# Kernel tuning notes

Measured on AMD Instinct MI355X. Metric: run time of the kernel, lower is better.

## Reference

```python
import jax, jax.numpy as jnp
import numpy as np

LOC_SIZE, TIM_SIZE = 50000, 48
LOC_EMB, TIM_EMB = 512, 32
IN = LOC_EMB + TIM_EMB  # 544
HID = 1024
SEQ, TGT = 4096, 1024


def _gru(x, Wih, Whh, bih, bhh):
    """PyTorch-convention GRU over [S, IN] -> [S, HID], h0 = 0."""
    gi = x @ Wih.T + bih  # [S, 3H] precomputed input gates
    H = Whh.shape[1]

    def step(h, gi_t):
        gh = Whh @ h + bhh
        i_r, i_z, i_n = jnp.split(gi_t, 3)
        h_r, h_z, h_n = jnp.split(gh, 3)
        r = jax.nn.sigmoid(i_r + h_r)
        z = jax.nn.sigmoid(i_z + h_z)
        n = jnp.tanh(i_n + r * h_n)
        h_new = (1.0 - z) * n + z * h
        return h_new, h_new

    _, hs = jax.lax.scan(step, jnp.zeros((H,), x.dtype), gi)
    return hs


def setup_inputs() -> dict:
    key = jax.random.key(0)
    ks = jax.random.split(key, 16)
    s = 0.02
    inp = {
        "loc": jax.random.randint(ks[0], (SEQ, 1), 0, LOC_SIZE),
        "tim": jax.random.randint(ks[1], (SEQ, 1), 0, TIM_SIZE),
        "target_len": TGT,
        "emb_loc": jax.random.normal(ks[2], (LOC_SIZE, LOC_EMB), jnp.float32) * s,
        "emb_tim": jax.random.normal(ks[3], (TIM_SIZE, TIM_EMB), jnp.float32) * s,
        "Wih_enc": jax.random.normal(ks[4], (3 * HID, IN), jnp.float32) * s,
        "Whh_enc": jax.random.normal(ks[5], (3 * HID, HID), jnp.float32) * s,
        "bih_enc": jnp.zeros((3 * HID,), jnp.float32),
        "bhh_enc": jnp.zeros((3 * HID,), jnp.float32),
        "Wih_dec": jax.random.normal(ks[6], (3 * HID, IN), jnp.float32) * s,
        "Whh_dec": jax.random.normal(ks[7], (3 * HID, HID), jnp.float32) * s,
        "bih_dec": jnp.zeros((3 * HID,), jnp.float32),
        "bhh_dec": jnp.zeros((3 * HID,), jnp.float32),
        "W_fc": jax.random.normal(ks[8], (LOC_SIZE, 2 * HID), jnp.float32) * s,
        "b_fc": jnp.zeros((LOC_SIZE,), jnp.float32),
    }
    return inp


def reference(loc, tim, target_len, emb_loc, emb_tim,
              Wih_enc, Whh_enc, bih_enc, bhh_enc,
              Wih_dec, Whh_dec, bih_dec, bhh_dec,
              W_fc, b_fc):
    # embeddings, batch dim of 1 squeezed: [S, IN]
    x = jnp.concatenate([emb_loc[loc[:, 0]], emb_tim[tim[:, 0]]], axis=1)
    # dropout is identity in eval mode
    hidden_history = _gru(x[:-target_len], Wih_enc, Whh_enc, bih_enc, bhh_enc)  # [S-T, H]
    hidden_state = _gru(x[-target_len:], Wih_dec, Whh_dec, bih_dec, bhh_dec)    # [T, H]
    # 'dot' attention: fused GEMM + row softmax (replaces the O(T*S) python loop)
    energies = hidden_state @ hidden_history.T                                   # [T, S-T]
    attn_weights = jax.nn.softmax(energies, axis=-1)
    context = attn_weights @ hidden_history                                      # [T, H]
    out = jnp.concatenate([hidden_state, context], axis=1)                       # [T, 2H]
    y = out @ W_fc.T + b_fc                                                      # [T, LOC_SIZE]
    return jax.nn.log_softmax(y, axis=-1)
```

## Files before the change

kernel.cpp:

```cpp
#include <hip/hip_runtime.h>
#include <hip/hip_bf16.h>
#include <cstdint>

typedef __attribute__((ext_vector_type(4))) float floatx4;
typedef __attribute__((ext_vector_type(8))) __bf16 bf16x8;
typedef __attribute__((ext_vector_type(4))) __bf16 bf16x4;
typedef unsigned long long u64t;

#define HID    1024
#define SEQ    4096
#define TGT    1024
#define ENC_T  3072
#define IN_DIM 544
#define NCLS   50000

__global__ __launch_bounds__(128) void embed_kernel(
    const int* __restrict__ loc, const int* __restrict__ tim,
    const float* __restrict__ el, const float* __restrict__ et,
    float* __restrict__ x) {
  int row = blockIdx.x, t = threadIdx.x;
  int li = loc[row], ti = tim[row];
  float4 v = *(const float4*)(el + (size_t)li * 512 + t * 4);
  *(float4*)(x + (size_t)row * IN_DIM + t * 4) = v;
  if (t < 8) {
    float4 w = *(const float4*)(et + (size_t)ti * 32 + t * 4);
    *(float4*)(x + (size_t)row * IN_DIM + 512 + t * 4) = w;
  }
}

#define BK  64
#define LDT 72

__global__ __launch_bounds__(256) void gemm_nt(
    const float* __restrict__ A, int lda,
    const float* __restrict__ B, int ldb,
    float* __restrict__ C, int ldc,
    const float* __restrict__ bias,
    int M, int N, int K) {
  __shared__ __bf16 As[128 * LDT];
  __shared__ __bf16 Bs[128 * LDT];
  const int tid = threadIdx.x;
  const int bm = blockIdx.x * 128, bn = blockIdx.y * 128;
  const int wave = tid >> 6, lane = tid & 63;
  const int wm = (wave & 1) * 64, wn = (wave >> 1) * 64;
  const int fr = lane & 15;
  const int kq = (lane >> 4) * 8;

  floatx4 acc[4][4];
#pragma unroll
  for (int i = 0; i < 4; i++)
#pragma unroll
    for (int j = 0; j < 4; j++) acc[i][j] = (floatx4){0.f, 0.f, 0.f, 0.f};

  const int nkt = (K + BK - 1) / BK;
  for (int kt = 0; kt < nkt; ++kt) {
    const int k0 = kt * BK;
#pragma unroll
    for (int i = 0; i < 8; i++) {
      int flat = tid + i * 256;
      int r = flat >> 4;
      int c4 = (flat & 15) * 4;
      float4 va = {0, 0, 0, 0}, vb = {0, 0, 0, 0};
      if (k0 + c4 < K) {
        va = *(const float4*)(A + (size_t)(bm + r) * lda + k0 + c4);
        if (bn + r < N) vb = *(const float4*)(B + (size_t)(bn + r) * ldb + k0 + c4);
      }
      *(bf16x4*)(As + r * LDT + c4) =
          (bf16x4){(__bf16)va.x, (__bf16)va.y, (__bf16)va.z, (__bf16)va.w};
      *(bf16x4*)(Bs + r * LDT + c4) =
          (bf16x4){(__bf16)vb.x, (__bf16)vb.y, (__bf16)vb.z, (__bf16)vb.w};
    }
    __syncthreads();
#pragma unroll
    for (int kh = 0; kh < 2; ++kh) {
      const int kf = kh * 32 + kq;
      bf16x8 af[4], bfr[4];
#pragma unroll
      for (int i = 0; i < 4; i++) {
        af[i]  = *(const bf16x8*)(As + (wm + i * 16 + fr) * LDT + kf);
        bfr[i] = *(const bf16x8*)(Bs + (wn + i * 16 + fr) * LDT + kf);
      }
#pragma unroll
      for (int mi = 0; mi < 4; mi++)
#pragma unroll
        for (int ni = 0; ni < 4; ni++)
          acc[mi][ni] = __builtin_amdgcn_mfma_f32_16x16x32_bf16(
              af[mi], bfr[ni], acc[mi][ni], 0, 0, 0);
    }
    __syncthreads();
  }

  const int em = (lane >> 4) * 4;
#pragma unroll
  for (int mi = 0; mi < 4; mi++) {
#pragma unroll
    for (int ni = 0; ni < 4; ni++) {
      int gn = bn + wn + ni * 16 + fr;
      if (gn < N) {
        float bv = bias ? bias[gn] : 0.f;
        int gm = bm + wm + mi * 16 + em;
#pragma unroll
        for (int r2 = 0; r2 < 4; r2++)
          C[(size_t)(gm + r2) * ldc + gn] = acc[mi][ni][r2] + bv;
      }
    }
  }
}

#define SC_WGS 128

__device__ __forceinline__ float flo(unsigned int u) {
  return __builtin_bit_cast(float, u << 16);
}
__device__ __forceinline__ float fhi(unsigned int u) {
  return __builtin_bit_cast(float, u & 0xffff0000u);
}

__global__ __launch_bounds__(256) void scan_kernel(
    const float* __restrict__ Whh_e, const float* __restrict__ bhh_e, const float* __restrict__ gi_e,
    const float* __restrict__ Whh_d, const float* __restrict__ bhh_d, const float* __restrict__ gi_d,
    float* __restrict__ Hh, float* __restrict__ HhT, float* __restrict__ outcat,
    unsigned int* __restrict__ hbuf_e, unsigned int* __restrict__ hbuf_d) {
  const bool enc = blockIdx.x < SC_WGS;
  const int wid = enc ? blockIdx.x : (blockIdx.x - SC_WGS);
  const int T = enc ? ENC_T : TGT;
  const float* Whh = enc ? Whh_e : Whh_d;
  const float* bhh = enc ? bhh_e : bhh_d;
  const float* gi  = enc ? gi_e : gi_d;
  unsigned int* hbuf = enc ? hbuf_e : hbuf_d;

  __shared__ uint2 wrz[8 * 512];
  __shared__ unsigned int wnn[8 * 512];
  const int tid = threadIdx.x;

  for (int i = tid; i < 8 * 512; i += 256) {
    int el = i >> 9, k2 = i & 511;
    int rb = wid * 8 + el;
    float2 w0 = *(const float2*)(Whh + (size_t)(0 * HID + rb) * HID + 2 * k2);
    float2 w1 = *(const float2*)(Whh + (size_t)(1 * HID + rb) * HID + 2 * k2);
    float2 w2 = *(const float2*)(Whh + (size_t)(2 * HID + rb) * HID + 2 * k2);
    unsigned int p0 = (unsigned int)__builtin_bit_cast(unsigned short, (__bf16)w0.x) |
                      ((unsigned int)__builtin_bit_cast(unsigned short, (__bf16)w0.y) << 16);
    unsigned int p1 = (unsigned int)__builtin_bit_cast(unsigned short, (__bf16)w1.x) |
                      ((unsigned int)__builtin_bit_cast(unsigned short, (__bf16)w1.y) << 16);
    unsigned int p2 = (unsigned int)__builtin_bit_cast(unsigned short, (__bf16)w2.x) |
                      ((unsigned int)__builtin_bit_cast(unsigned short, (__bf16)w2.y) << 16);
    wrz[i] = make_uint2(p0, p1);
    wnn[i] = p2;
  }
  __syncthreads();

  const int l = tid & 63;
  const int w = tid >> 6;
  const int le0 = w * 2, le1 = le0 + 1;
  const int e0 = wid * 8 + le0;

  float bq = 0.f;
  if (l < 3) bq = bhh[l * HID + e0];
  else if (l >= 4 && l < 7) bq = bhh[(l - 4) * HID + (e0 + 1)];

  const uint2* wrz0 = wrz + le0 * 512;
  const uint2* wrz1 = wrz + le1 * 512;
  const unsigned int* wnn0 = wnn + le0 * 512;
  const unsigned int* wnn1 = wnn + le1 * 512;

  float h_own = 0.f;
  long budget = 1L << 21;

  for (int t = 0; t < T; ++t) {
    float gval = 0.f;
    if (l < 3) gval = gi[(size_t)t * 3072 + l * HID + e0];
    else if (l >= 4 && l < 7) gval = gi[(size_t)t * 3072 + (l - 4) * HID + (e0 + 1)];

    const u64t* hp = (const u64t*)(hbuf + ((t + 1) & 1) * HID);
    const unsigned int tlo = (unsigned int)t;
    float ar0, az0, an0, ar1, az1, an1;
    for (;;) {
      u64t hv[8];
#pragma unroll
      for (int j = 0; j < 8; ++j)
        hv[j] = __hip_atomic_load(hp + l + 64 * j, __ATOMIC_RELAXED, __HIP_MEMORY_SCOPE_AGENT);
      bool ok = true;
      ar0 = az0 = an0 = ar1 = az1 = an1 = 0.f;
#pragma unroll
      for (int j = 0; j < 8; ++j) {
        unsigned int w0 = (unsigned int)hv[j];
        unsigned int w1 = (unsigned int)(hv[j] >> 32);
        ok &= ((w0 >> 16) >= tlo) & ((w1 >> 16) >= tlo);
        float h0 = flo(w0);
        float h1 = flo(w1);
        int i = l + 64 * j;
        uint2 u0 = wrz0[i];
        unsigned int n0 = wnn0[i];
        uint2 u1 = wrz1[i];
        unsigned int n1 = wnn1[i];
        ar0 += flo(u0.x) * h0 + fhi(u0.x) * h1;
        az0 += flo(u0.y) * h0 + fhi(u0.y) * h1;
        an0 += flo(n0) * h0 + fhi(n0) * h1;
        ar1 += flo(u1.x) * h0 + fhi(u1.x) * h1;
        az1 += flo(u1.y) * h0 + fhi(u1.y) * h1;
        an1 += flo(n1) * h0 + fhi(n1) * h1;
      }
      if (__all(ok)) break;
      if (--budget < 0) break;
    }
#pragma unroll
    for (int o = 32; o; o >>= 1) {
      ar0 += __shfl_xor(ar0, o); az0 += __shfl_xor(az0, o); an0 += __shfl_xor(an0, o);
      ar1 += __shfl_xor(ar1, o); az1 += __shfl_xor(az1, o); an1 += __shfl_xor(an1, o);
    }
    int base = (l & 1) * 4;
    float i_r = __shfl(gval, base + 0);
    float i_z = __shfl(gval, base + 1);
    float i_n = __shfl(gval, base + 2);
    float b_r = __shfl(bq, base + 0);
    float b_z = __shfl(bq, base + 1);
    float b_n = __shfl(bq, base + 2);
    if (l < 2) {
      float sr = l ? ar1 : ar0;
      float sz = l ? az1 : az0;
      float sn = l ? an1 : an0;
      int e = e0 + l;
      float r = 1.f / (1.f + expf(-(i_r + sr + b_r)));
      float z = 1.f / (1.f + expf(-(i_z + sz + b_z)));
      float nn2 = tanhf(i_n + r * (sn + b_n));
      float hnew = (1.f - z) * nn2 + z * h_own;
      h_own = hnew;
      unsigned int pk = ((unsigned int)(t + 1) << 16) |
                        (unsigned int)__builtin_bit_cast(unsigned short, (__bf16)hnew);
      __hip_atomic_store(&hbuf[(t & 1) * HID + e], pk,
                         __ATOMIC_RELAXED, __HIP_MEMORY_SCOPE_AGENT);
      if (enc) {
        Hh[(size_t)t * HID + e] = hnew;
        HhT[(size_t)e * ENC_T + t] = hnew;
      } else {
        outcat[(size_t)t * 2048 + e] = hnew;
      }
    }
  }
}

__device__ __forceinline__ float wave_max(float v) {
#pragma unroll
  for (int o = 32; o; o >>= 1) v = fmaxf(v, __shfl_xor(v, o));
  return v;
}
__device__ __forceinline__ float wave_sum(float v) {
#pragma unroll
  for (int o = 32; o; o >>= 1) v += __shfl_xor(v, o);
  return v;
}

__global__ __launch_bounds__(256) void softmax_kernel(float* __restrict__ E) {
  __shared__ float red[4];
  int row = blockIdx.x;
  float* p = E + (size_t)row * ENC_T;
  int tid = threadIdx.x, wave = tid >> 6;
  float v[12];
  float m = -3.4e38f;
#pragma unroll
  for (int j = 0; j < 12; j++) { v[j] = p[tid + j * 256]; m = fmaxf(m, v[j]); }
  m = wave_max(m);
  if ((tid & 63) == 0) red[wave] = m;
  __syncthreads();
  m = fmaxf(fmaxf(red[0], red[1]), fmaxf(red[2], red[3]));
  __syncthreads();
  float s = 0.f;
#pragma unroll
  for (int j = 0; j < 12; j++) { v[j] = expf(v[j] - m); s += v[j]; }
  s = wave_sum(s);
  if ((tid & 63) == 0) red[wave] = s;
  __syncthreads();
  s = red[0] + red[1] + red[2] + red[3];
  float inv = 1.f / s;
#pragma unroll
  for (int j = 0; j < 12; j++) p[tid + j * 256] = v[j] * inv;
}

__global__ __launch_bounds__(256) void lse_kernel(const float* __restrict__ Y,
                                                  float* __restrict__ lse) {
  __shared__ float red[4];
  int row = blockIdx.x;
  const float* p = Y + (size_t)row * NCLS;
  int tid = threadIdx.x, wave = tid >> 6;
  float m = -3.4e38f;
  for (int c = tid; c < NCLS; c += 256) m = fmaxf(m, p[c]);
  m = wave_max(m);
  if ((tid & 63) == 0) red[wave] = m;
  __syncthreads();
  m = fmaxf(fmaxf(red[0], red[1]), fmaxf(red[2], red[3]));
  __syncthreads();
  float s = 0.f;
  for (int c = tid; c < NCLS; c += 256) s += expf(p[c] - m);
  s = wave_sum(s);
  if ((tid & 63) == 0) red[wave] = s;
  __syncthreads();
  if (tid == 0) lse[row] = m + logf(red[0] + red[1] + red[2] + red[3]);
}

__global__ __launch_bounds__(256) void sub_kernel(float* __restrict__ Y,
                                                  const float* __restrict__ lse) {
  const unsigned total = (unsigned)TGT * (NCLS / 4);
  unsigned stride = gridDim.x * 256;
  for (unsigned i = blockIdx.x * 256 + threadIdx.x; i < total; i += stride) {
    unsigned row = i / (NCLS / 4);
    float l = lse[row];
    float4 v = ((float4*)Y)[i];
    v.x -= l; v.y -= l; v.z -= l; v.w -= l;
    ((float4*)Y)[i] = v;
  }
}

extern "C" void kernel_launch(void* const* d_in, const int* in_sizes, int n_in,
                              void* d_out, int out_size, void* d_ws, size_t ws_size,
                              hipStream_t stream) {
  const int*   loc     = (const int*)d_in[0];
  const int*   tim     = (const int*)d_in[1];
  const float* emb_loc = (const float*)d_in[3];
  const float* emb_tim = (const float*)d_in[4];
  const float* Wih_e   = (const float*)d_in[5];
  const float* Whh_e   = (const float*)d_in[6];
  const float* bih_e   = (const float*)d_in[7];
  const float* bhh_e   = (const float*)d_in[8];
  const float* Wih_d   = (const float*)d_in[9];
  const float* Whh_d   = (const float*)d_in[10];
  const float* bih_d   = (const float*)d_in[11];
  const float* bhh_d   = (const float*)d_in[12];
  const float* W_fc    = (const float*)d_in[13];
  const float* b_fc    = (const float*)d_in[14];
  float* out = (float*)d_out;

  float* ws = (float*)d_ws;
  unsigned int* hbuf_e = (unsigned int*)ws;
  unsigned int* hbuf_d = (unsigned int*)(ws + 2048);
  float* lse    = ws + 4096;
  float* x      = ws + 5120;
  float* gi_e   = x + (size_t)SEQ * IN_DIM;
  float* gi_d   = gi_e + (size_t)ENC_T * 3072;
  float* Hh     = gi_d + (size_t)TGT * 3072;
  float* HhT    = Hh + (size_t)ENC_T * HID;
  float* outcat = HhT + (size_t)HID * ENC_T;
  float* energ  = outcat + (size_t)TGT * 2048;

  hipMemsetAsync(d_ws, 0, 4096 * sizeof(float), stream);

  embed_kernel<<<SEQ, 128, 0, stream>>>(loc, tim, emb_loc, emb_tim, x);

  gemm_nt<<<dim3(ENC_T / 128, 3072 / 128), 256, 0, stream>>>(
      x, IN_DIM, Wih_e, IN_DIM, gi_e, 3072, bih_e, ENC_T, 3072, IN_DIM);
  gemm_nt<<<dim3(TGT / 128, 3072 / 128), 256, 0, stream>>>(
      x + (size_t)ENC_T * IN_DIM, IN_DIM, Wih_d, IN_DIM, gi_d, 3072, bih_d, TGT, 3072, IN_DIM);

  scan_kernel<<<2 * SC_WGS, 256, 0, stream>>>(Whh_e, bhh_e, gi_e, Whh_d, bhh_d, gi_d,
                                              Hh, HhT, outcat, hbuf_e, hbuf_d);

  gemm_nt<<<dim3(TGT / 128, ENC_T / 128), 256, 0, stream>>>(
      outcat, 2048, Hh, HID, energ, ENC_T, nullptr, TGT, ENC_T, HID);
  softmax_kernel<<<TGT, 256, 0, stream>>>(energ);
  gemm_nt<<<dim3(TGT / 128, HID / 128), 256, 0, stream>>>(
      energ, ENC_T, HhT, ENC_T, outcat + HID, 2048, nullptr, TGT, HID, ENC_T);

  gemm_nt<<<dim3(TGT / 128, (NCLS + 127) / 128), 256, 0, stream>>>(
      outcat, 2048, W_fc, 2048, out, NCLS, b_fc, TGT, NCLS, 2048);

  lse_kernel<<<TGT, 256, 0, stream>>>(out, lse);
  sub_kernel<<<4096, 256, 0, stream>>>(out, lse);
}
```

Baseline: 16.99 ms.

## Add aggregator workgroup publishing per-step epoch counter for scan synchronization

Adds an extra workgroup to the persistent GRU scan kernel. It polls the tagged hidden-state buffers, computes the minimum completed step across all elements, and publishes it to 16 replicated epoch counters. Scan workgroups then spin on a single epoch word before loading the full hidden vector, instead of repeatedly reloading all 8 tagged words per lane. This aims to cut global polling traffic and contention, but adds a hop of latency per step through the aggregator. It also relies on the extra block being co-resident with the others.

Measured after the change: 14.20 ms. -16.4%, faster.

```diff
diff --git a/kernel.cpp b/kernel.cpp
--- a/kernel.cpp
+++ b/kernel.cpp
@@ -120,7 +120,43 @@
     const float* __restrict__ Whh_e, const float* __restrict__ bhh_e, const float* __restrict__ gi_e,
     const float* __restrict__ Whh_d, const float* __restrict__ bhh_d, const float* __restrict__ gi_d,
     float* __restrict__ Hh, float* __restrict__ HhT, float* __restrict__ outcat,
-    unsigned int* __restrict__ hbuf_e, unsigned int* __restrict__ hbuf_d) {
+    unsigned int* __restrict__ hbuf_e, unsigned int* __restrict__ hbuf_d,
+    unsigned int* __restrict__ epoch) {
+  const int tid = threadIdx.x;
+
+  if (blockIdx.x == 2 * SC_WGS) {
+    const int w = tid >> 6, l = tid & 63;
+    if (w < 2) {
+      const u64t* sp = (const u64t*)(w == 0 ? hbuf_e : hbuf_d);
+      unsigned int* ep = epoch + (w == 0 ? 0 : 256);
+      const unsigned int Ta = (w == 0) ? ENC_T : TGT;
+      unsigned int last = 0;
+      long arounds = 1L << 22;
+      while (last < Ta && --arounds > 0) {
+        unsigned int mn = 0xffffffffu;
+#pragma unroll
+        for (int j = 0; j < 8; ++j) {
+          u64t a = __hip_atomic_load(sp + l + 64 * j, __ATOMIC_RELAXED, __HIP_MEMORY_SCOPE_AGENT);
+          u64t b = __hip_atomic_load(sp + 512 + l + 64 * j, __ATOMIC_RELAXED, __HIP_MEMORY_SCOPE_AGENT);
+          unsigned int s0 = max((unsigned int)a >> 16, (unsigned int)b >> 16);
+          unsigned int s1 = max((unsigned int)(a >> 32) >> 16, (unsigned int)(b >> 32) >> 16);
+          mn = min(mn, min(s0, s1));
+        }
+#pragma unroll
+        for (int o = 32; o; o >>= 1) {
+          unsigned int m2 = (unsigned int)__shfl_xor((int)mn, o);
+          mn = min(mn, m2);
+        }
+        if (mn > last) {
+          last = mn;
+          if (l < 16)
+            __hip_atomic_store(ep + l * 16, mn, __ATOMIC_RELAXED, __HIP_MEMORY_SCOPE_AGENT);
+        }
+      }
+    }
+    return;
+  }
+
   const bool enc = blockIdx.x < SC_WGS;
   const int wid = enc ? blockIdx.x : (blockIdx.x - SC_WGS);
   const int T = enc ? ENC_T : TGT;
@@ -128,10 +164,10 @@
   const float* bhh = enc ? bhh_e : bhh_d;
   const float* gi  = enc ? gi_e : gi_d;
   unsigned int* hbuf = enc ? hbuf_e : hbuf_d;
+  const unsigned int* myep = epoch + (enc ? 0 : 256) + (blockIdx.x & 15) * 16;
 
   __shared__ uint2 wrz[8 * 512];
   __shared__ unsigned int wnn[8 * 512];
-  const int tid = threadIdx.x;
 
   for (int i = tid; i < 8 * 512; i += 256) {
     int el = i >> 9, k2 = i & 511;
@@ -171,6 +207,14 @@
     float gval = 0.f;
     if (l < 3) gval = gi[(size_t)t * 3072 + l * HID + e0];
     else if (l >= 4 && l < 7) gval = gi[(size_t)t * 3072 + (l - 4) * HID + (e0 + 1)];
+
+    if (t > 0) {
+      while (__hip_atomic_load(myep, __ATOMIC_RELAXED, __HIP_MEMORY_SCOPE_AGENT)
+             < (unsigned int)t) {
+        if (--budget < 0) break;
+      }
+      asm volatile("" ::: "memory");
+    }
 
     const u64t* hp = (const u64t*)(hbuf + ((t + 1) & 1) * HID);
     const unsigned int tlo = (unsigned int)t;
@@ -333,8 +377,9 @@
   float* ws = (float*)d_ws;
   unsigned int* hbuf_e = (unsigned int*)ws;
   unsigned int* hbuf_d = (unsigned int*)(ws + 2048);
-  float* lse    = ws + 4096;
-  float* x      = ws + 5120;
+  unsigned int* epoch  = (unsigned int*)(ws + 4096);
+  float* lse    = ws + 4608;
+  float* x      = ws + 5632;
   float* gi_e   = x + (size_t)SEQ * IN_DIM;
   float* gi_d   = gi_e + (size_t)ENC_T * 3072;
   float* Hh     = gi_d + (size_t)TGT * 3072;
@@ -342,7 +387,7 @@
   float* outcat = HhT + (size_t)HID * ENC_T;
   float* energ  = outcat + (size_t)TGT * 2048;
 
-  hipMemsetAsync(d_ws, 0, 4096 * sizeof(float), stream);
+  hipMemsetAsync(d_ws, 0, 4608 * sizeof(float), stream);
 
   embed_kernel<<<SEQ, 128, 0, stream>>>(loc, tim, emb_loc, emb_tim, x);
 
@@ -351,8 +396,8 @@
   gemm_nt<<<dim3(TGT / 128, 3072 / 128), 256, 0, stream>>>(
       x + (size_t)ENC_T * IN_DIM, IN_DIM, Wih_d, IN_DIM, gi_d, 3072, bih_d, TGT, 3072, IN_DIM);
 
-  scan_kernel<<<2 * SC_WGS, 256, 0, stream>>>(Whh_e, bhh_e, gi_e, Whh_d, bhh_d, gi_d,
-                                              Hh, HhT, outcat, hbuf_e, hbuf_d);
+  scan_kernel<<<2 * SC_WGS + 1, 256, 0, stream>>>(Whh_e, bhh_e, gi_e, Whh_d, bhh_d, gi_d,
+                                                  Hh, HhT, outcat, hbuf_e, hbuf_d, epoch);
 
   gemm_nt<<<dim3(TGT / 128, ENC_T / 128), 256, 0, stream>>>(
       outcat, 2048, Hh, HID, energ, ENC_T, nullptr, TGT, ENC_T, HID);
```
